# Optimization experiments

Measured on AMD Instinct MI355X. Metric: run time of the kernel, lower is better.

The kernel has to match this reference:

```python
import jax, jax.numpy as jnp
import numpy as np

B, N, DIM_IN, DIM_OUT, CHEB_K, EMBED_DIM = 64, 2048, 64, 64, 3, 10


def setup_inputs() -> dict:
    key = jax.random.key(0)
    k1, k2, k3, k4 = jax.random.split(key, 4)
    x = jax.random.normal(k1, (B, N, DIM_IN), dtype=jnp.float32)
    node_embeddings = jax.random.normal(k2, (N, EMBED_DIM), dtype=jnp.float32)
    # xavier-normal-like init for the pools
    w_std = (2.0 / (EMBED_DIM * CHEB_K * DIM_IN + DIM_OUT)) ** 0.5
    b_std = (2.0 / (EMBED_DIM + DIM_OUT)) ** 0.5
    weights_pool = jax.random.normal(k3, (EMBED_DIM, CHEB_K, DIM_IN, DIM_OUT), dtype=jnp.float32) * w_std
    bias_pool = jax.random.normal(k4, (EMBED_DIM, DIM_OUT), dtype=jnp.float32) * b_std
    return {"x": x, "node_embeddings": node_embeddings,
            "weights_pool": weights_pool, "bias_pool": bias_pool,
            "cheb_k": CHEB_K}


def reference(x, node_embeddings, weights_pool, bias_pool, cheb_k):
    n = node_embeddings.shape[0]
    # adaptive adjacency: softmax(relu(E E^T)) over neighbors
    supports = jax.nn.softmax(jax.nn.relu(node_embeddings @ node_embeddings.T), axis=1)
    # Chebyshev polynomial supports: T0 = I, T1 = A, Tk = 2 A T_{k-1} - T_{k-2}
    support_set = [jnp.eye(n, dtype=supports.dtype), supports]
    for _ in range(2, cheb_k):
        support_set.append(2.0 * supports @ support_set[-1] - support_set[-2])
    supports_k = jnp.stack(support_set, axis=0)  # [K, N, N]
    # per-node weights and bias synthesized from node embeddings
    weights = jnp.einsum('nd,dkio->nkio', node_embeddings, weights_pool)  # [N, K, I, O]
    bias = node_embeddings @ bias_pool                                    # [N, O]
    # graph convolution
    x_g = jnp.einsum('knm,bmc->bnkc', supports_k, x)                      # [B, N, K, I]
    out = jnp.einsum('bnki,nkio->bno', x_g, weights) + bias               # [B, N, O]
    return out
```

## Files before the change

kernel.cpp:

```cpp
#include <hip/hip_runtime.h>

#define NN 2048
#define BB 64
#define CC 64
#define ED 10
#define KK 3
#define JJ (BB * CC)

typedef unsigned short ushort_t;
typedef __attribute__((ext_vector_type(8))) short short8;
typedef __attribute__((ext_vector_type(4))) float f32x4;

typedef const __attribute__((address_space(1))) unsigned* gptr_t;
typedef __attribute__((address_space(3))) unsigned* lptr_t;
typedef __attribute__((address_space(3))) ushort_t* lsptr_t;
typedef const __attribute__((address_space(3))) short8* ls8_t;

static __device__ __forceinline__ ushort_t f2bf(float f) {
    union { float f; unsigned u; } x{f};
    unsigned r = x.u + 0x7FFF + ((x.u >> 16) & 1);
    return (ushort_t)(r >> 16);
}
static __device__ __forceinline__ float bf2f(ushort_t h) {
    union { unsigned u; float f; } x;
    x.u = ((unsigned)h) << 16;
    return x.f;
}

__global__ __launch_bounds__(256) void prep_kernel(const float* __restrict__ E,
                                                   const float* __restrict__ x,
                                                   const float* __restrict__ Wp,
                                                   ushort_t* __restrict__ Ab,
                                                   ushort_t* __restrict__ xT,
                                                   ushort_t* __restrict__ xN,
                                                   ushort_t* __restrict__ WpT) {
    const int bid = blockIdx.x;
    const int tid = threadIdx.x;

    __shared__ float tb[64][68];
    __shared__ float red[8];

    if (bid < NN) {
        const int n = bid;
        float en[ED];
#pragma unroll
        for (int d = 0; d < ED; ++d) en[d] = E[n * ED + d];

        float sv[NN / 256];
        float lmax = 0.0f;
#pragma unroll
        for (int j = 0; j < NN / 256; ++j) {
            const int m = tid + j * 256;
            const float* Em = E + m * ED;
            float dot = 0.0f;
#pragma unroll
            for (int d = 0; d < ED; ++d) dot += en[d] * Em[d];
            float s = fmaxf(dot, 0.0f);
            sv[j] = s;
            lmax = fmaxf(lmax, s);
        }
#pragma unroll
        for (int off = 32; off > 0; off >>= 1) lmax = fmaxf(lmax, __shfl_down(lmax, off, 64));
        if ((tid & 63) == 0) red[tid >> 6] = lmax;
        __syncthreads();
        const float bmax = fmaxf(fmaxf(red[0], red[1]), fmaxf(red[2], red[3]));

        float lsum = 0.0f;
#pragma unroll
        for (int j = 0; j < NN / 256; ++j) {
            sv[j] = __expf(sv[j] - bmax);
            lsum += sv[j];
        }
#pragma unroll
        for (int off = 32; off > 0; off >>= 1) lsum += __shfl_down(lsum, off, 64);
        if ((tid & 63) == 0) red[4 + (tid >> 6)] = lsum;
        __syncthreads();
        const float inv = 1.0f / (red[4] + red[5] + red[6] + red[7]);

#pragma unroll
        for (int j = 0; j < NN / 256; ++j) {
            Ab[(size_t)n * NN + tid + j * 256] = f2bf(sv[j] * inv);
        }
    } else if (bid < 2 * NN) {
        const int t = bid - NN;
        const int n0 = (t & 31) * 64;
        const int b = t >> 5;

#pragma unroll
        for (int l = 0; l < 4; ++l) {
            const int idx = tid + l * 256;
            const int nn = idx >> 4;
            const int c4 = (idx & 15) << 2;
            const float4 v = *(const float4*)(x + ((size_t)b * NN + n0 + nn) * CC + c4);
            tb[c4 + 0][nn] = v.x;
            tb[c4 + 1][nn] = v.y;
            tb[c4 + 2][nn] = v.z;
            tb[c4 + 3][nn] = v.w;
        }
        __syncthreads();

#pragma unroll
        for (int l = 0; l < 2; ++l) {
            const int idx = tid + l * 256;
            const int c = idx >> 3;
            const int ch = (idx & 7) << 3;
            ushort_t pack[8];
#pragma unroll
            for (int e = 0; e < 8; ++e) pack[e] = f2bf(tb[c][ch + e]);
            *(float4*)(xT + (size_t)(b * 64 + c) * NN + n0 + ch) = *(float4*)pack;
        }
#pragma unroll
        for (int l = 0; l < 2; ++l) {
            const int idx = tid + l * 256;
            const int nn = idx >> 3;
            const int cg = (idx & 7) << 3;
            ushort_t pack[8];
#pragma unroll
            for (int e = 0; e < 8; ++e) pack[e] = f2bf(tb[cg + e][nn]);
            *(float4*)(xN + (size_t)(n0 + nn) * JJ + b * 64 + cg) = *(float4*)pack;
        }
    } else {
        const int dk = bid - 2 * NN;
        const float* src = Wp + (size_t)dk * CC * CC;

#pragma unroll
        for (int l = 0; l < 4; ++l) {
            const int idx = tid + l * 256;
            const int i = idx >> 4;
            const int o4 = (idx & 15) << 2;
            const float4 v = *(const float4*)(src + i * CC + o4);
            tb[o4 + 0][i] = v.x;
            tb[o4 + 1][i] = v.y;
            tb[o4 + 2][i] = v.z;
            tb[o4 + 3][i] = v.w;
        }
        __syncthreads();

#pragma unroll
        for (int l = 0; l < 2; ++l) {
            const int idx = tid + l * 256;
            const int o = idx >> 3;
            const int ic = (idx & 7) << 3;
            ushort_t pack[8];
#pragma unroll
            for (int e = 0; e < 8; ++e) pack[e] = f2bf(tb[o][ic + e]);
            *(float4*)(WpT + (size_t)dk * CC * CC + o * CC + ic) = *(float4*)pack;
        }
    }
}

#define STAGE_A(bp, kt) do {                                                                \
    __builtin_amdgcn_global_load_lds(                                                       \
        (gptr_t)(srcA + (size_t)(kt) * 64),                                                 \
        (lptr_t)&(bp)[dstoff], 16, 0, 0);                                                   \
    __builtin_amdgcn_global_load_lds(                                                       \
        (gptr_t)(srcA + (size_t)64 * NN + (size_t)(kt) * 64),                               \
        (lptr_t)&(bp)[4096 + dstoff], 16, 0, 0);                                            \
} while (0)

#define STAGE_B(bp, h, kt) do {                                                             \
    __builtin_amdgcn_global_load_lds(                                                       \
        (gptr_t)(srcB + (size_t)((h) * 2) * 64 * NN + (size_t)(kt) * 64),                   \
        (lptr_t)&(bp)[8192 + (h) * 8192 + dstoff], 16, 0, 0);                               \
    __builtin_amdgcn_global_load_lds(                                                       \
        (gptr_t)(srcB + (size_t)((h) * 2 + 1) * 64 * NN + (size_t)(kt) * 64),               \
        (lptr_t)&(bp)[8192 + (h) * 8192 + 4096 + dstoff], 16, 0, 0);                        \
} while (0)

#define LDA_ALL(bp) do {                                                                    \
    _Pragma("unroll") for (int mi_ = 0; mi_ < 4; ++mi_)                                     \
    _Pragma("unroll") for (int ks_ = 0; ks_ < 2; ++ks_)                                     \
        a[mi_][ks_] = *(ls8_t)&(bp)[(aRG + mi_) * 1024 + ks_ * 512 + rdofs];                \
} while (0)

#define LDB_H(bp, h) do {                                                                   \
    _Pragma("unroll") for (int nn_ = 0; nn_ < 2; ++nn_)                                     \
    _Pragma("unroll") for (int ks_ = 0; ks_ < 2; ++ks_)                                     \
        b[(h) * 2 + nn_][ks_] =                                                             \
            *(ls8_t)&(bp)[8192 + (bRG + (h) * 2 + nn_) * 1024 + ks_ * 512 + rdofs];         \
} while (0)

#define MFMA_C(c) do {                                                                      \
    __builtin_amdgcn_s_setprio(1);                                                          \
    _Pragma("unroll") for (int mi_ = 0; mi_ < 4; ++mi_)                                     \
    _Pragma("unroll") for (int nn_ = 0; nn_ < 2; ++nn_) {                                   \
        acc[mi_][(c) * 2 + nn_] = __builtin_amdgcn_mfma_f32_16x16x32_bf16(                  \
            a[mi_][0], b[(c) * 2 + nn_][0], acc[mi_][(c) * 2 + nn_], 0, 0, 0);              \
        acc[mi_][(c) * 2 + nn_] = __builtin_amdgcn_mfma_f32_16x16x32_bf16(                  \
            a[mi_][1], b[(c) * 2 + nn_][1], acc[mi_][(c) * 2 + nn_], 0, 0, 0);              \
    }                                                                                       \
    __builtin_amdgcn_s_setprio(0);                                                          \
} while (0)

template <int MODE>
__global__ __launch_bounds__(512, 2) void gemm_roll(const ushort_t* __restrict__ A,
                                                    const ushort_t* __restrict__ Bt,
                                                    const ushort_t* __restrict__ Zn,
                                                    ushort_t* __restrict__ Ct,
                                                    ushort_t* __restrict__ Cn) {
    int bid = blockIdx.x;
    bid = (bid & 7) * 32 + (bid >> 3);
    const int bx = bid & 15;
    const int by = bid >> 4;
    const int j0 = bx * 256;
    const int m0 = by * 128;

    const int tid = threadIdx.x;
    const int w = tid >> 6;
    const int lane = tid & 63;
    const int l16 = lane & 15;
    const int quad = lane >> 4;
    const int wm = (w >> 2) * 64;
    const int wn = (w & 3) * 64;
    const int aRG = (w >> 2) * 4;
    const int bRG = (w & 3) * 4;
    const int rdofs = l16 * 32 + ((quad * 8) ^ ((l16 & 8) * 2));

    const int r16s = lane >> 2;
    const int cx = (lane & 3) ^ ((r16s >> 3) << 1);
    const int rowbase = (w >> 1) * 16 + r16s;
    const int kofs = (w & 1) * 32 + cx * 8;
    const ushort_t* srcA = A + (size_t)(m0 + rowbase) * NN + kofs;
    const ushort_t* srcB = Bt + (size_t)(j0 + rowbase) * NN + kofs;
    const int dstoff = tid * 8;

    __shared__ ushort_t lds[3][24576];

    lsptr_t p0 = (lsptr_t)&lds[0][0];
    lsptr_t p1 = (lsptr_t)&lds[1][0];
    lsptr_t p2 = (lsptr_t)&lds[2][0];

    f32x4 acc[4][4];
#pragma unroll
    for (int mi = 0; mi < 4; ++mi)
#pragma unroll
        for (int ni = 0; ni < 4; ++ni) acc[mi][ni] = (f32x4){0.f, 0.f, 0.f, 0.f};

    short8 a[4][2], b[4][2];

    STAGE_A(p0, 0); STAGE_B(p0, 0, 0); STAGE_B(p0, 1, 0);
    STAGE_A(p1, 1); STAGE_B(p1, 0, 1); STAGE_B(p1, 1, 1);

#pragma unroll 1
    for (int t = 0; t < 32; ++t) {
        if (t) MFMA_C(1);
        if (t < 31) { asm volatile("s_waitcnt vmcnt(6)" ::: "memory"); }
        else        { asm volatile("s_waitcnt vmcnt(0)" ::: "memory"); }
        __builtin_amdgcn_sched_barrier(0);
        __builtin_amdgcn_s_barrier();

        LDA_ALL(p0); LDB_H(p0, 0);
        const bool stg = (t < 30);
        if (stg) { STAGE_A(p2, t + 2); STAGE_B(p2, 0, t + 2); }
        asm volatile("s_waitcnt lgkmcnt(0)" ::: "memory");
        __builtin_amdgcn_sched_barrier(0);
        MFMA_C(0);
        LDB_H(p0, 1);
        if (stg) STAGE_B(p2, 1, t + 2);
        __builtin_amdgcn_sched_barrier(0);

        lsptr_t tp = p0; p0 = p1; p1 = p2; p2 = tp;
    }
    MFMA_C(1);

#pragma unroll
    for (int mi = 0; mi < 4; ++mi) {
#pragma unroll
        for (int ji = 0; ji < 4; ++ji) {
            const int j = j0 + wn + ji * 16 + l16;
            const int mb = m0 + wm + mi * 16 + quad * 4;
            if (MODE == 0) {
                ushort_t o[4];
#pragma unroll
                for (int r = 0; r < 4; ++r) o[r] = f2bf(acc[mi][ji][r]);
                *(unsigned long long*)(Ct + (size_t)j * NN + mb) = *(unsigned long long*)o;
#pragma unroll
                for (int r = 0; r < 4; ++r) Cn[(size_t)(mb + r) * JJ + j] = o[r];
            } else {
#pragma unroll
                for (int r = 0; r < 4; ++r) {
                    const float z = bf2f(Zn[(size_t)(mb + r) * JJ + j]);
                    Cn[(size_t)(mb + r) * JJ + j] = f2bf(2.0f * acc[mi][ji][r] - z);
                }
            }
        }
    }
}

#undef STAGE_A
#undef STAGE_B
#undef LDA_ALL
#undef LDB_H
#undef MFMA_C

#define XLD 200
__global__ __launch_bounds__(256) void out_kernel(const float* __restrict__ E,
                                                  const ushort_t* __restrict__ WpT,
                                                  const float* __restrict__ bp,
                                                  const ushort_t* __restrict__ xN,
                                                  const ushort_t* __restrict__ y1N,
                                                  const ushort_t* __restrict__ y2N,
                                                  float* __restrict__ out) {
    const int n = blockIdx.x;
    const int tid = threadIdx.x;

    __shared__ ushort_t xg[BB * XLD];
    __shared__ ushort_t Wt[CC * XLD];
    __shared__ float en_s[ED];
    __shared__ float bias_s[CC];

    if (tid < ED) en_s[tid] = E[n * ED + tid];
    __syncthreads();

    float en[ED];
#pragma unroll
    for (int d = 0; d < ED; ++d) en[d] = en_s[d];

    if (tid < CC) {
        float bsum = 0.0f;
#pragma unroll
        for (int d = 0; d < ED; ++d) bsum += en[d] * bp[d * CC + tid];
        bias_s[tid] = bsum;
    }

#pragma unroll
    for (int k = 0; k < KK; ++k) {
        const ushort_t* src = (k == 0) ? xN : (k == 1) ? y1N : y2N;
        const float4* srow = (const float4*)(src + (size_t)n * JJ);
        for (int idx = tid; idx < JJ / 8; idx += 256) {
            *(float4*)&xg[(idx >> 3) * XLD + k * 64 + ((idx & 7) << 3)] = srow[idx];
        }
    }

    for (int t = tid; t < CC * 24; t += 256) {
        const int o = t / 24;
        const int kc = t % 24;
        const int k = kc >> 3;
        const int ic = (kc & 7) << 3;
        float s[8];
#pragma unroll
        for (int e = 0; e < 8; ++e) s[e] = 0.0f;
#pragma unroll
        for (int d = 0; d < ED; ++d) {
            const float4 wv4 = *(const float4*)(WpT + ((size_t)(d * KK + k) * CC + o) * CC + ic);
            const ushort_t* wp = (const ushort_t*)&wv4;
#pragma unroll
            for (int e = 0; e < 8; ++e) s[e] += en[d] * bf2f(wp[e]);
        }
        ushort_t pack[8];
#pragma unroll
        for (int e = 0; e < 8; ++e) pack[e] = f2bf(s[e]);
        *(float4*)&Wt[o * XLD + k * 64 + ic] = *(float4*)pack;
    }
    __syncthreads();

    const int lane = tid & 63;
    const int l16 = lane & 15;
    const int quad = lane >> 4;
    const int bm = (tid >> 6) * 16;

    f32x4 acc[4];
#pragma unroll
    for (int ji = 0; ji < 4; ++ji) acc[ji] = (f32x4){0.f, 0.f, 0.f, 0.f};

#pragma unroll
    for (int kc = 0; kc < 6; ++kc) {
        const short8 av = *(const short8*)&xg[(bm + l16) * XLD + kc * 32 + quad * 8];
#pragma unroll
        for (int ji = 0; ji < 4; ++ji) {
            const short8 bv = *(const short8*)&Wt[(ji * 16 + l16) * XLD + kc * 32 + quad * 8];
            acc[ji] = __builtin_amdgcn_mfma_f32_16x16x32_bf16(av, bv, acc[ji], 0, 0, 0);
        }
    }

#pragma unroll
    for (int ji = 0; ji < 4; ++ji) {
        const int o = ji * 16 + l16;
        const float bo = bias_s[o];
#pragma unroll
        for (int r = 0; r < 4; ++r) {
            const int b = bm + quad * 4 + r;
            out[((size_t)b * NN + n) * CC + o] = acc[ji][r] + bo;
        }
    }
}
#undef XLD

extern "C" void kernel_launch(void* const* d_in, const int* in_sizes, int n_in,
                              void* d_out, int out_size, void* d_ws, size_t ws_size,
                              hipStream_t stream) {
    const float* x  = (const float*)d_in[0];
    const float* E  = (const float*)d_in[1];
    const float* Wp = (const float*)d_in[2];
    const float* bp = (const float*)d_in[3];

    ushort_t* Ab  = (ushort_t*)d_ws;
    ushort_t* xT  = Ab + (size_t)NN * NN;
    ushort_t* xN  = xT + (size_t)JJ * NN;
    ushort_t* y1T = xN + (size_t)NN * JJ;
    ushort_t* y1N = y1T + (size_t)JJ * NN;
    ushort_t* y2N = y1N + (size_t)NN * JJ;
    ushort_t* WpT = y2N + (size_t)NN * JJ;
    float* out = (float*)d_out;

    prep_kernel<<<2 * NN + ED * KK, 256, 0, stream>>>(E, x, Wp, Ab, xT, xN, WpT);
    gemm_roll<0><<<256, 512, 0, stream>>>(Ab, xT, nullptr, y1T, y1N);
    gemm_roll<1><<<256, 512, 0, stream>>>(Ab, y1T, xN, nullptr, y2N);
    out_kernel<<<NN, 256, 0, stream>>>(E, WpT, bp, xN, y1N, y2N, out);
}
```

Baseline: 204.4 us.

## Move Chebyshev recurrence into output kernel and read activations directly from global

The second GEMM now writes only the raw A·y1 product into the freed xT buffer instead of reading xN and computing 2·A·y1 − x in its epilogue. The output kernel applies the 2·y2 − x correction on the fly from register-held x fragments. That kernel also drops the shared-memory staging of x/y1/y2 and the bias shared array, loading MFMA operands straight from global memory. The aim is to cut global traffic and LDS usage, at the cost of an extra bf16 rounding step and uncoalesced 16-byte fragment loads in the output kernel. The embedding dot products in prep are also vectorised to float2 loads.

New measurement: 200.1 us. -2.1%, faster.

```diff
diff --git a/kernel.cpp b/kernel.cpp
--- a/kernel.cpp
+++ b/kernel.cpp
@@ -51,10 +51,13 @@
 #pragma unroll
         for (int j = 0; j < NN / 256; ++j) {
             const int m = tid + j * 256;
-            const float* Em = E + m * ED;
+            const float2* Em2 = (const float2*)(E + m * ED);
             float dot = 0.0f;
 #pragma unroll
-            for (int d = 0; d < ED; ++d) dot += en[d] * Em[d];
+            for (int d2 = 0; d2 < ED / 2; ++d2) {
+                const float2 v = Em2[d2];
+                dot += en[2 * d2] * v.x + en[2 * d2 + 1] * v.y;
+            }
             float s = fmaxf(dot, 0.0f);
             sv[j] = s;
             lmax = fmaxf(lmax, s);
@@ -195,7 +198,6 @@
 template <int MODE>
 __global__ __launch_bounds__(512, 2) void gemm_roll(const ushort_t* __restrict__ A,
                                                     const ushort_t* __restrict__ Bt,
-                                                    const ushort_t* __restrict__ Zn,
                                                     ushort_t* __restrict__ Ct,
                                                     ushort_t* __restrict__ Cn) {
     int bid = blockIdx.x;
@@ -269,20 +271,14 @@
         for (int ji = 0; ji < 4; ++ji) {
             const int j = j0 + wn + ji * 16 + l16;
             const int mb = m0 + wm + mi * 16 + quad * 4;
+            ushort_t o[4];
+#pragma unroll
+            for (int r = 0; r < 4; ++r) o[r] = f2bf(acc[mi][ji][r]);
             if (MODE == 0) {
-                ushort_t o[4];
-#pragma unroll
-                for (int r = 0; r < 4; ++r) o[r] = f2bf(acc[mi][ji][r]);
                 *(unsigned long long*)(Ct + (size_t)j * NN + mb) = *(unsigned long long*)o;
-#pragma unroll
-                for (int r = 0; r < 4; ++r) Cn[(size_t)(mb + r) * JJ + j] = o[r];
-            } else {
-#pragma unroll
-                for (int r = 0; r < 4; ++r) {
-                    const float z = bf2f(Zn[(size_t)(mb + r) * JJ + j]);
-                    Cn[(size_t)(mb + r) * JJ + j] = f2bf(2.0f * acc[mi][ji][r] - z);
-                }
             }
+#pragma unroll
+            for (int r = 0; r < 4; ++r) Cn[(size_t)(mb + r) * JJ + j] = o[r];
         }
     }
 }
@@ -299,38 +295,16 @@
                                                   const float* __restrict__ bp,
                                                   const ushort_t* __restrict__ xN,
                                                   const ushort_t* __restrict__ y1N,
-                                                  const ushort_t* __restrict__ y2N,
+                                                  const ushort_t* __restrict__ y2r,
                                                   float* __restrict__ out) {
     const int n = blockIdx.x;
     const int tid = threadIdx.x;
 
-    __shared__ ushort_t xg[BB * XLD];
     __shared__ ushort_t Wt[CC * XLD];
-    __shared__ float en_s[ED];
-    __shared__ float bias_s[CC];
-
-    if (tid < ED) en_s[tid] = E[n * ED + tid];
-    __syncthreads();
 
     float en[ED];
 #pragma unroll
-    for (int d = 0; d < ED; ++d) en[d] = en_s[d];
-
-    if (tid < CC) {
-        float bsum = 0.0f;
-#pragma unroll
-        for (int d = 0; d < ED; ++d) bsum += en[d] * bp[d * CC + tid];
-        bias_s[tid] = bsum;
-    }
-
-#pragma unroll
-    for (int k = 0; k < KK; ++k) {
-        const ushort_t* src = (k == 0) ? xN : (k == 1) ? y1N : y2N;
-        const float4* srow = (const float4*)(src + (size_t)n * JJ);
-        for (int idx = tid; idx < JJ / 8; idx += 256) {
-            *(float4*)&xg[(idx >> 3) * XLD + k * 64 + ((idx & 7) << 3)] = srow[idx];
-        }
-    }
+    for (int d = 0; d < ED; ++d) en[d] = E[n * ED + d];
 
     for (int t = tid; t < CC * 24; t += 256) {
         const int o = t / 24;
@@ -359,13 +333,45 @@
     const int quad = lane >> 4;
     const int bm = (tid >> 6) * 16;
 
+    float bo[4];
+#pragma unroll
+    for (int ji = 0; ji < 4; ++ji) {
+        float s = 0.0f;
+#pragma unroll
+        for (int d = 0; d < ED; ++d) s += en[d] * bp[d * CC + ji * 16 + l16];
+        bo[ji] = s;
+    }
+
     f32x4 acc[4];
 #pragma unroll
     for (int ji = 0; ji < 4; ++ji) acc[ji] = (f32x4){0.f, 0.f, 0.f, 0.f};
 
+    const int rb = (bm + l16) * 64 + quad * 8;
+    const ushort_t* xrow = xN + (size_t)n * JJ + rb;
+    const ushort_t* y1row = y1N + (size_t)n * JJ + rb;
+    const ushort_t* y2row = y2r + (size_t)n * JJ + rb;
+
+    short8 ax[2];
+
 #pragma unroll
     for (int kc = 0; kc < 6; ++kc) {
-        const short8 av = *(const short8*)&xg[(bm + l16) * XLD + kc * 32 + quad * 8];
+        const int h32 = (kc & 1) * 32;
+        short8 av;
+        if (kc < 2) {
+            ax[kc] = *(const short8*)(xrow + h32);
+            av = ax[kc];
+        } else if (kc < 4) {
+            av = *(const short8*)(y1row + h32);
+        } else {
+            const short8 v2 = *(const short8*)(y2row + h32);
+            const ushort_t* p2 = (const ushort_t*)&v2;
+            const ushort_t* px = (const ushort_t*)&ax[kc & 1];
+            ushort_t pk[8];
+#pragma unroll
+            for (int e = 0; e < 8; ++e)
+                pk[e] = f2bf(2.0f * bf2f(p2[e]) - bf2f(px[e]));
+            av = *(short8*)pk;
+        }
 #pragma unroll
         for (int ji = 0; ji < 4; ++ji) {
             const short8 bv = *(const short8*)&Wt[(ji * 16 + l16) * XLD + kc * 32 + quad * 8];
@@ -376,11 +382,10 @@
 #pragma unroll
     for (int ji = 0; ji < 4; ++ji) {
         const int o = ji * 16 + l16;
-        const float bo = bias_s[o];
 #pragma unroll
         for (int r = 0; r < 4; ++r) {
             const int b = bm + quad * 4 + r;
-            out[((size_t)b * NN + n) * CC + o] = acc[ji][r] + bo;
+            out[((size_t)b * NN + n) * CC + o] = acc[ji][r] + bo[ji];
         }
     }
 }
@@ -399,12 +404,12 @@
     ushort_t* xN  = xT + (size_t)JJ * NN;
     ushort_t* y1T = xN + (size_t)NN * JJ;
     ushort_t* y1N = y1T + (size_t)JJ * NN;
-    ushort_t* y2N = y1N + (size_t)NN * JJ;
-    ushort_t* WpT = y2N + (size_t)NN * JJ;
+    ushort_t* WpT = y1N + (size_t)NN * JJ;
+    ushort_t* y2r = xT;
     float* out = (float*)d_out;
 
     prep_kernel<<<2 * NN + ED * KK, 256, 0, stream>>>(E, x, Wp, Ab, xT, xN, WpT);
-    gemm_roll<0><<<256, 512, 0, stream>>>(Ab, xT, nullptr, y1T, y1N);
-    gemm_roll<1><<<256, 512, 0, stream>>>(Ab, y1T, xN, nullptr, y2N);
-    out_kernel<<<NN, 256, 0, stream>>>(E, WpT, bp, xN, y1N, y2N, out);
-}
+    gemm_roll<0><<<256, 512, 0, stream>>>(Ab, xT, y1T, y1N);
+    gemm_roll<1><<<256, 512, 0, stream>>>(Ab, y1T, nullptr, y2r);
+    out_kernel<<<NN, 256, 0, stream>>>(E, WpT, bp, xN, y1N, y2r, out);
+}
```
